# Kernel optimization log

Hardware: AMD Instinct MI355X
Metric: run time of the kernel (lower is better)

Reference implementation:

```python
import jax, jax.numpy as jnp
import numpy as np

BATCH = 1048576
HIDDEN = 64


def setup_inputs() -> dict:
    key = jax.random.key(0)
    ks = jax.random.split(key, 6)
    # inputs must be positive because one branch transform is log
    x = jax.random.uniform(ks[0], (BATCH, 10), dtype=jnp.float32, minval=0.01, maxval=1.0)
    gate_logits = jax.random.normal(ks[1], (4,), dtype=jnp.float32)
    # torch Linear(2, H): y = x @ W.T + b ; store already-transposed weights
    w1 = jax.random.normal(ks[2], (2, HIDDEN), dtype=jnp.float32) * (1.0 / np.sqrt(2.0))
    b1 = jax.random.normal(ks[3], (HIDDEN,), dtype=jnp.float32) * 0.01
    w2 = jax.random.normal(ks[4], (HIDDEN, 1), dtype=jnp.float32) * (1.0 / np.sqrt(HIDDEN))
    b2 = jax.random.normal(ks[5], (1,), dtype=jnp.float32) * 0.01
    return {"x": x, "gate_logits": gate_logits, "w1": w1, "b1": b1, "w2": w2, "b2": b2}


def reference(x, gate_logits, w1, b1, w2, b2):
    # gate index shared across batch and all 5 items
    idx = jnp.argmax(gate_logits)
    # apply the 4 transforms to all 10 features at once: (B, 10, 4)
    trans = jnp.stack([x, jnp.log(x), jnp.exp(x), jnp.sin(x)], axis=-1)
    sel = jnp.take(trans, idx, axis=-1)          # (B, 10)
    wi = sel[:, :5]                              # (B, 5) weights
    pi = sel[:, 5:]                              # (B, 5) profits
    inp = jnp.stack([wi, pi], axis=-1)           # (B, 5, 2)
    h = jax.nn.relu(jnp.einsum('bif,fh->bih', inp, w1) + b1)   # (B, 5, H)
    out = jnp.einsum('bih,ho->bio', h, w2) + b2                # (B, 5, 1)
    return out[..., 0]                           # (B, 5)
```

## Files before the change

kernel.cpp:

```cpp
#include <hip/hip_runtime.h>

#define BATCH 1048576
#define HIDDEN 64

__global__ __launch_bounds__(256) void simplenn_kernel(
    const float* __restrict__ x,
    const float* __restrict__ gate,
    const float* __restrict__ w1,
    const float* __restrict__ b1,
    const float* __restrict__ w2,
    const float* __restrict__ b2,
    float* __restrict__ out)
{
    const int t = blockIdx.x * blockDim.x + threadIdx.x;

    float g0 = gate[0], g1 = gate[1], g2 = gate[2], g3 = gate[3];
    int idx = 0; float gm = g0;
    if (g1 > gm) { gm = g1; idx = 1; }
    if (g2 > gm) { gm = g2; idx = 2; }
    if (g3 > gm) { gm = g3; idx = 3; }

    const float4* xv = (const float4*)(x + (size_t)t * 20);
    float4 q0 = xv[0], q1 = xv[1], q2 = xv[2], q3 = xv[3], q4 = xv[4];
    float v[20] = { q0.x,q0.y,q0.z,q0.w, q1.x,q1.y,q1.z,q1.w,
                    q2.x,q2.y,q2.z,q2.w, q3.x,q3.y,q3.z,q3.w,
                    q4.x,q4.y,q4.z,q4.w };

    if (idx == 1) {
        #pragma unroll
        for (int j = 0; j < 20; ++j) v[j] = __logf(v[j]);
    } else if (idx == 2) {
        #pragma unroll
        for (int j = 0; j < 20; ++j) v[j] = __expf(v[j]);
    } else if (idx == 3) {
        #pragma unroll
        for (int j = 0; j < 20; ++j) v[j] = __sinf(v[j]);
    }

    float acc[10];
    const float bias2 = b2[0];
    #pragma unroll
    for (int i = 0; i < 10; ++i) acc[i] = bias2;

    #pragma unroll 8
    for (int h = 0; h < HIDDEN; ++h) {
        const float a  = w1[h];
        const float c  = w1[HIDDEN + h];
        const float bb = b1[h];
        const float w  = w2[h];
        #pragma unroll
        for (int i = 0; i < 5; ++i) {
            float t0 = fmaf(v[i],      a, fmaf(v[i + 5],  c, bb));
            float t1 = fmaf(v[10 + i], a, fmaf(v[15 + i], c, bb));
            t0 = fmaxf(t0, 0.f);
            t1 = fmaxf(t1, 0.f);
            acc[i]     = fmaf(t0, w, acc[i]);
            acc[5 + i] = fmaf(t1, w, acc[5 + i]);
        }
    }

    float2* o = (float2*)(out + (size_t)t * 10);
    o[0] = make_float2(acc[0], acc[1]);
    o[1] = make_float2(acc[2], acc[3]);
    o[2] = make_float2(acc[4], acc[5]);
    o[3] = make_float2(acc[6], acc[7]);
    o[4] = make_float2(acc[8], acc[9]);
}

extern "C" void kernel_launch(void* const* d_in, const int* in_sizes, int n_in,
                              void* d_out, int out_size, void* d_ws, size_t ws_size,
                              hipStream_t stream) {
    const float* x    = (const float*)d_in[0];
    const float* gate = (const float*)d_in[1];
    const float* w1   = (const float*)d_in[2];
    const float* b1   = (const float*)d_in[3];
    const float* w2   = (const float*)d_in[4];
    const float* b2   = (const float*)d_in[5];
    float* out = (float*)d_out;

    const int n_threads = BATCH / 2;
    const int block = 256;
    const int grid = n_threads / block;
    simplenn_kernel<<<grid, block, 0, stream>>>(x, gate, w1, b1, w2, b2, out);
}
```

Before: 117.4 us.

## Compute hidden layer in packed fp16 with weights staged in LDS

Each thread packs its two batch rows' inputs into fp16 pairs and runs the 64-unit hidden layer with packed half-precision FMA and max, so one instruction covers both rows. Weights are converted to duplicated fp16 pairs in shared memory once per block, replacing the per-iteration global loads. Partial sums are accumulated in fp16 over 16-unit segments and then added into fp32, which limits but does not remove the precision loss. The risk is accuracy: log inputs near zero and exp values feed fp16 rounding and could exceed the tolerance.

After: 108.3 us. 1.08x faster.

```diff
diff --git a/kernel.cpp b/kernel.cpp
--- a/kernel.cpp
+++ b/kernel.cpp
@@ -2,6 +2,12 @@
 
 #define BATCH 1048576
 #define HIDDEN 64
+
+typedef _Float16 h2 __attribute__((ext_vector_type(2)));
+
+static __device__ __forceinline__ h2 pack2(float a, float b) {
+    return __builtin_bit_cast(h2, __builtin_amdgcn_cvt_pkrtz(a, b));
+}
 
 __global__ __launch_bounds__(256) void simplenn_kernel(
     const float* __restrict__ x,
@@ -12,7 +18,16 @@
     const float* __restrict__ b2,
     float* __restrict__ out)
 {
-    const int t = blockIdx.x * blockDim.x + threadIdx.x;
+    __shared__ __align__(16) h2 lw[HIDDEN][4];
+
+    const int tid = threadIdx.x;
+    if (tid < HIDDEN) {
+        float a = w1[tid], c = w1[HIDDEN + tid], bb = b1[tid], w = w2[tid];
+        lw[tid][0] = pack2(a, a);
+        lw[tid][1] = pack2(c, c);
+        lw[tid][2] = pack2(bb, bb);
+        lw[tid][3] = pack2(w, w);
+    }
 
     float g0 = gate[0], g1 = gate[1], g2 = gate[2], g3 = gate[3];
     int idx = 0; float gm = g0;
@@ -20,6 +35,7 @@
     if (g2 > gm) { gm = g2; idx = 2; }
     if (g3 > gm) { gm = g3; idx = 3; }
 
+    const int t = blockIdx.x * blockDim.x + tid;
     const float4* xv = (const float4*)(x + (size_t)t * 20);
     float4 q0 = xv[0], q1 = xv[1], q2 = xv[2], q3 = xv[3], q4 = xv[4];
     float v[20] = { q0.x,q0.y,q0.z,q0.w, q1.x,q1.y,q1.z,q1.w,
@@ -37,34 +53,51 @@
         for (int j = 0; j < 20; ++j) v[j] = __sinf(v[j]);
     }
 
-    float acc[10];
+    __syncthreads();
+
+    h2 wiP[5], piP[5];
+    #pragma unroll
+    for (int i = 0; i < 5; ++i) {
+        wiP[i] = pack2(v[i],     v[10 + i]);
+        piP[i] = pack2(v[5 + i], v[15 + i]);
+    }
+
+    const h2 zero = { (_Float16)0, (_Float16)0 };
     const float bias2 = b2[0];
+    float accx[5], accy[5];
     #pragma unroll
-    for (int i = 0; i < 10; ++i) acc[i] = bias2;
+    for (int i = 0; i < 5; ++i) { accx[i] = bias2; accy[i] = bias2; }
 
-    #pragma unroll 8
-    for (int h = 0; h < HIDDEN; ++h) {
-        const float a  = w1[h];
-        const float c  = w1[HIDDEN + h];
-        const float bb = b1[h];
-        const float w  = w2[h];
+    for (int seg = 0; seg < 4; ++seg) {
+        h2 acc[5];
+        #pragma unroll
+        for (int i = 0; i < 5; ++i) acc[i] = zero;
+
+        #pragma unroll
+        for (int k = 0; k < 16; ++k) {
+            const int h = seg * 16 + k;
+            h2 aa = lw[h][0], cc = lw[h][1], bp = lw[h][2], wp = lw[h][3];
+            #pragma unroll
+            for (int i = 0; i < 5; ++i) {
+                h2 pre = __builtin_elementwise_fma(piP[i], cc, bp);
+                pre    = __builtin_elementwise_fma(wiP[i], aa, pre);
+                pre    = __builtin_elementwise_max(pre, zero);
+                acc[i] = __builtin_elementwise_fma(pre, wp, acc[i]);
+            }
+        }
         #pragma unroll
         for (int i = 0; i < 5; ++i) {
-            float t0 = fmaf(v[i],      a, fmaf(v[i + 5],  c, bb));
-            float t1 = fmaf(v[10 + i], a, fmaf(v[15 + i], c, bb));
-            t0 = fmaxf(t0, 0.f);
-            t1 = fmaxf(t1, 0.f);
-            acc[i]     = fmaf(t0, w, acc[i]);
-            acc[5 + i] = fmaf(t1, w, acc[5 + i]);
+            accx[i] += (float)acc[i].x;
+            accy[i] += (float)acc[i].y;
         }
     }
 
     float2* o = (float2*)(out + (size_t)t * 10);
-    o[0] = make_float2(acc[0], acc[1]);
-    o[1] = make_float2(acc[2], acc[3]);
-    o[2] = make_float2(acc[4], acc[5]);
-    o[3] = make_float2(acc[6], acc[7]);
-    o[4] = make_float2(acc[8], acc[9]);
+    o[0] = make_float2(accx[0], accx[1]);
+    o[1] = make_float2(accx[2], accx[3]);
+    o[2] = make_float2(accx[4], accy[0]);
+    o[3] = make_float2(accy[1], accy[2]);
+    o[4] = make_float2(accy[3], accy[4]);
 }
 
 extern "C" void kernel_launch(void* const* d_in, const int* in_sizes, int n_in,
```

## Compute hidden layer in packed fp16 with weights staged in LDS

Applied to the files above, without the earlier changes.

Packs the first-layer weights, biases and second-layer weights into fp16 pairs in shared memory. The inner loop now handles two hidden units per step using packed fp16 FMA, max, and fdot2 accumulation into fp32. This roughly halves the ALU instruction count of a compute-bound loop. The cost is lower precision in the pre-activation values, plus an added barrier and LDS reads.

Measured after the change: 105.5 us. 10.2% less time.

```diff
diff --git a/kernel.cpp b/kernel.cpp
--- a/kernel.cpp
+++ b/kernel.cpp
@@ -2,6 +2,12 @@
 
 #define BATCH 1048576
 #define HIDDEN 64
+
+typedef _Float16 h2 __attribute__((ext_vector_type(2)));
+
+static __device__ __forceinline__ h2 pack2(float a, float b) {
+    return __builtin_bit_cast(h2, __builtin_amdgcn_cvt_pkrtz(a, b));
+}
 
 __global__ __launch_bounds__(256) void simplenn_kernel(
     const float* __restrict__ x,
@@ -12,7 +18,16 @@
     const float* __restrict__ b2,
     float* __restrict__ out)
 {
-    const int t = blockIdx.x * blockDim.x + threadIdx.x;
+    __shared__ __align__(16) h2 lw[HIDDEN / 2][4];
+
+    const int tid = threadIdx.x;
+    if (tid < HIDDEN / 2) {
+        const int h0 = 2 * tid, h1 = 2 * tid + 1;
+        lw[tid][0] = pack2(w1[h0],          w1[h1]);
+        lw[tid][1] = pack2(w1[HIDDEN + h0], w1[HIDDEN + h1]);
+        lw[tid][2] = pack2(b1[h0],          b1[h1]);
+        lw[tid][3] = pack2(w2[h0],          w2[h1]);
+    }
 
     float g0 = gate[0], g1 = gate[1], g2 = gate[2], g3 = gate[3];
     int idx = 0; float gm = g0;
@@ -20,6 +35,7 @@
     if (g2 > gm) { gm = g2; idx = 2; }
     if (g3 > gm) { gm = g3; idx = 3; }
 
+    const int t = blockIdx.x * blockDim.x + tid;
     const float4* xv = (const float4*)(x + (size_t)t * 20);
     float4 q0 = xv[0], q1 = xv[1], q2 = xv[2], q3 = xv[3], q4 = xv[4];
     float v[20] = { q0.x,q0.y,q0.z,q0.w, q1.x,q1.y,q1.z,q1.w,
@@ -37,25 +53,32 @@
         for (int j = 0; j < 20; ++j) v[j] = __sinf(v[j]);
     }
 
+    __syncthreads();
+
+    h2 wiB[10], piB[10];
+    #pragma unroll
+    for (int i = 0; i < 5; ++i) {
+        wiB[i]     = pack2(v[i],      v[i]);
+        piB[i]     = pack2(v[5 + i],  v[5 + i]);
+        wiB[5 + i] = pack2(v[10 + i], v[10 + i]);
+        piB[5 + i] = pack2(v[15 + i], v[15 + i]);
+    }
+
+    const h2 zero = { (_Float16)0, (_Float16)0 };
+    const float bias2 = b2[0];
     float acc[10];
-    const float bias2 = b2[0];
     #pragma unroll
-    for (int i = 0; i < 10; ++i) acc[i] = bias2;
+    for (int j = 0; j < 10; ++j) acc[j] = bias2;
 
     #pragma unroll 8
-    for (int h = 0; h < HIDDEN; ++h) {
-        const float a  = w1[h];
-        const float c  = w1[HIDDEN + h];
-        const float bb = b1[h];
-        const float w  = w2[h];
+    for (int hp = 0; hp < HIDDEN / 2; ++hp) {
+        const h2 aa = lw[hp][0], cc = lw[hp][1], bb = lw[hp][2], ww = lw[hp][3];
         #pragma unroll
-        for (int i = 0; i < 5; ++i) {
-            float t0 = fmaf(v[i],      a, fmaf(v[i + 5],  c, bb));
-            float t1 = fmaf(v[10 + i], a, fmaf(v[15 + i], c, bb));
-            t0 = fmaxf(t0, 0.f);
-            t1 = fmaxf(t1, 0.f);
-            acc[i]     = fmaf(t0, w, acc[i]);
-            acc[5 + i] = fmaf(t1, w, acc[5 + i]);
+        for (int j = 0; j < 10; ++j) {
+            h2 pre = __builtin_elementwise_fma(piB[j], cc, bb);
+            pre    = __builtin_elementwise_fma(wiB[j], aa, pre);
+            pre    = __builtin_elementwise_max(pre, zero);
+            acc[j] = __builtin_amdgcn_fdot2(pre, ww, acc[j], false);
         }
     }
 
```
